# Performance work log

Measured on AMD Instinct MI355X. Metric: run time of the kernel, lower is better.

## Reference

```python
import jax, jax.numpy as jnp
import numpy as np
import math

B, L, D = 4, 4096, 1024
PI = math.pi
LN_EPS = 1e-5


def setup_inputs() -> dict:
    key = jax.random.key(0)
    ks = jax.random.split(key, 16)
    s = 1.0 / math.sqrt(D)
    inp = {
        "x": jax.random.normal(ks[0], (B, L, D), dtype=jnp.float32),
        # Linear weights stored as [in, out] (torch W.T)
        "Wk": jax.random.normal(ks[1], (D, D), dtype=jnp.float32) * s,
        "bk": jnp.zeros((D,), dtype=jnp.float32),
        "Wq": jax.random.normal(ks[2], (D, D), dtype=jnp.float32) * s,
        "bq": jnp.zeros((D,), dtype=jnp.float32),
        "Wv": jax.random.normal(ks[3], (D, D), dtype=jnp.float32) * s,
        "bv": jnp.zeros((D,), dtype=jnp.float32),
        "ln_g": jnp.ones((D,), dtype=jnp.float32),
        "ln_b": jnp.zeros((D,), dtype=jnp.float32),
        "Wo": jax.random.normal(ks[4], (D, D), dtype=jnp.float32) * s,
        "bo": jnp.zeros((D,), dtype=jnp.float32),
        "Wg1": jax.random.normal(ks[5], (D, D // 4), dtype=jnp.float32) * s,
        "bg1": jnp.zeros((D // 4,), dtype=jnp.float32),
        "Wg2": jax.random.normal(ks[6], (D // 4, 1), dtype=jnp.float32) * (2.0 / math.sqrt(D)),
        "bg2": jnp.zeros((1,), dtype=jnp.float32),
        "pos_phases": jax.random.normal(ks[7], (L, D), dtype=jnp.float32) * PI,
    }
    return inp


def _layernorm(x, g, b):
    mu = jnp.mean(x, axis=-1, keepdims=True)
    var = jnp.var(x, axis=-1, keepdims=True)
    return (x - mu) * jax.lax.rsqrt(var + LN_EPS) * g + b


def reference(x, Wk, bk, Wq, bq, Wv, bv, ln_g, ln_b, Wo, bo, Wg1, bg1, Wg2, bg2, pos_phases):
    # dropout is identity in eval mode
    key_phases = jnp.tanh(x @ Wk + bk) * PI          # [B,L,D]
    query_phases = jnp.tanh(x @ Wq + bq) * PI        # [B,L,D]
    V = x @ Wv + bv                                   # [B,L,D]

    cos_k, sin_k = jnp.cos(key_phases), jnp.sin(key_phases)
    cos_q, sin_q = jnp.cos(query_phases), jnp.sin(query_phases)

    mem_real = jnp.cumsum(V * cos_k, axis=1)
    mem_imag = jnp.cumsum(V * sin_k, axis=1)
    content_retrieved = mem_real * cos_q + mem_imag * sin_q

    pp = pos_phases[: x.shape[1]]                     # [L,D]
    cos_p, sin_p = jnp.cos(pp), jnp.sin(pp)
    pos_mem_real = jnp.cumsum(V * cos_p, axis=1)
    pos_mem_imag = jnp.cumsum(V * sin_p, axis=1)
    pos_retrieved = pos_mem_real * cos_p + pos_mem_imag * sin_p

    gate = jax.nn.sigmoid(jax.nn.gelu(x @ Wg1 + bg1) @ Wg2 + bg2)  # [B,L,1]
    combined = gate * content_retrieved + (1.0 - gate) * pos_retrieved

    positions = jnp.arange(1, x.shape[1] + 1, dtype=jnp.float32)
    norm = jnp.sqrt(positions)[None, :, None]
    out = _layernorm(combined / norm, ln_g, ln_b) @ Wo + bo
    return x + out
```

## Files before the change

### kernel.cpp

```cpp
#include <hip/hip_runtime.h>
#include <math.h>

#define B_ 4
#define L_ 4096
#define D_ 1024
#define DG_ 256
#define NC_ 128
#define CL_ 32
#define PI_F 3.14159265358979323846f
#define LN_EPS_F 1e-5f

typedef __attribute__((ext_vector_type(8))) _Float16 f16x8;
typedef __attribute__((ext_vector_type(8))) short s16x8;
typedef __attribute__((ext_vector_type(4))) short s16x4;
typedef __attribute__((ext_vector_type(4))) float f32x4;

__device__ inline short f2h(float f) { return __builtin_bit_cast(short, (_Float16)f); }
__device__ inline float h2f(short s) { return (float)__builtin_bit_cast(_Float16, s); }

__device__ inline float ftanh(float x) {
    float e = __expf(2.0f * x);
    return 1.0f - 2.0f / (e + 1.0f);
}
__device__ inline void fsincos(float x, float* s, float* c) {
    *s = __sinf(x); *c = __cosf(x);
}

__device__ inline void gld16(const void* g, void* l) {
    __builtin_amdgcn_global_load_lds(
        (const __attribute__((address_space(1))) unsigned int*)g,
        (__attribute__((address_space(3))) unsigned int*)l, 16, 0, 0);
}

__global__ __launch_bounds__(256)
void conv_x(const float* __restrict__ x, short* __restrict__ xh, int n8)
{
    int t = blockIdx.x * 256 + threadIdx.x;
    if (t >= n8) return;
    const float4* p = (const float4*)x + (size_t)t * 2;
    float4 a = p[0], b = p[1];
    s16x8 v;
    v[0] = f2h(a.x); v[1] = f2h(a.y); v[2] = f2h(a.z); v[3] = f2h(a.w);
    v[4] = f2h(b.x); v[5] = f2h(b.y); v[6] = f2h(b.z); v[7] = f2h(b.w);
    *(s16x8*)(xh + (size_t)t * 8) = v;
}

__global__ __launch_bounds__(256)
void convT(const float* __restrict__ W, short* __restrict__ Th, int N)
{
    __shared__ float tile[64][65];
    const int n0 = blockIdx.x * 64, k0 = blockIdx.y * 64;
    const int t = threadIdx.x;
    const int r = t >> 4, c4 = (t & 15) * 4;

    #pragma unroll
    for (int i = 0; i < 4; ++i) {
        float4 v = *(const float4*)&W[(size_t)(k0 + r + i * 16) * N + n0 + c4];
        tile[r + i * 16][c4 + 0] = v.x;
        tile[r + i * 16][c4 + 1] = v.y;
        tile[r + i * 16][c4 + 2] = v.z;
        tile[r + i * 16][c4 + 3] = v.w;
    }
    __syncthreads();
    #pragma unroll
    for (int i = 0; i < 4; ++i) {
        const int n = r + i * 16;
        s16x4 o;
        o[0] = f2h(tile[c4 + 0][n]);
        o[1] = f2h(tile[c4 + 1][n]);
        o[2] = f2h(tile[c4 + 2][n]);
        o[3] = f2h(tile[c4 + 3][n]);
        *(s16x4*)&Th[(size_t)(n0 + n) * 1024 + k0 + c4] = o;
    }
}

__device__ inline f16x8 ldf(const char* lds, int ofs, int r, int colb) {
    return *(const f16x8*)(lds + ofs + r * 128 + (colb ^ ((r & 7) << 4)));
}

#define STG(srcp, rbase, kt, lofs)                                              \
    gld16((const char*)(srcp) + (size_t)((rbase) + sr) * (size_t)(K * 2) +      \
              (kt) * 128 + sc,                                                  \
          lds + (lofs) + (w << 10))

#define MFMA_Q(MG, NG)                                                          \
    _Pragma("unroll") for (int i_ = 0; i_ < 4; ++i_)                            \
    _Pragma("unroll") for (int j_ = 0; j_ < 2; ++j_)                            \
    _Pragma("unroll") for (int kk_ = 0; kk_ < 2; ++kk_)                         \
        acc[(MG)*4 + i_][(NG)*2 + j_] = __builtin_amdgcn_mfma_f32_16x16x32_f16( \
            af[i_][kk_], bq[NG][j_][kk_], acc[(MG)*4 + i_][(NG)*2 + j_], 0, 0, 0);

#define SBAR() __builtin_amdgcn_sched_barrier(0)

template<int EPI, typename OT>
__global__ __launch_bounds__(512, 2)
void mgemm256(const short* __restrict__ A, const short* __restrict__ Bt,
              const float* __restrict__ X, OT* __restrict__ out0,
              short* __restrict__ out1, short* __restrict__ out2,
              const float* __restrict__ b0, const float* __restrict__ b1,
              const float* __restrict__ b2, int M, int N, int K)
{
    extern __shared__ char lds[];

    const int tid = threadIdx.x;
    const int w = tid >> 6, l = tid & 63;
    const int wr = w >> 2, wc = w & 3;
    const int fr = l & 15, kb = l >> 4;
    const int bm = blockIdx.x * 256, bn = blockIdx.y * 256;
    const int nt = K >> 6;

    const int p0 = tid * 16;
    const int sr = p0 >> 7;
    const int sc = (p0 & 127) ^ ((sr & 7) << 4);

    f32x4 acc[8][4] = {};
    f16x8 af[4][2];
    f16x8 bq[2][2][2];

    STG(A, bm +   0, 0, 0);             STG(A, bm + 128, 0, 16384);
    STG(A, bm +  64, 0, 8192);          STG(A, bm + 192, 0, 16384 + 8192);
    STG(Bt, bn +   0, 0, 32768);        STG(Bt, bn +  64, 0, 32768 + 8192);
    STG(Bt, bn + 128, 0, 32768 + 16384);STG(Bt, bn + 192, 0, 32768 + 16384 + 8192);
    STG(A, bm +   0, 1, 65536);         STG(A, bm + 128, 1, 65536 + 16384);
    STG(A, bm +  64, 1, 65536 + 8192);  STG(A, bm + 192, 1, 65536 + 16384 + 8192);
    STG(Bt, bn +   0, 1, 98304);        STG(Bt, bn +  64, 1, 98304 + 8192);
    STG(Bt, bn + 128, 1, 98304 + 16384);STG(Bt, bn + 192, 1, 98304 + 16384 + 8192);
    asm volatile("s_waitcnt vmcnt(8)" ::: "memory");
    SBAR(); __builtin_amdgcn_s_barrier(); SBAR();

    for (int t = 0; t < nt; ++t) {
        const int Ab = (t & 1) << 16, Bb = Ab + 32768;
        const int An = ((t & 1) ^ 1) << 16, Bn = An + 32768;
        const bool sNext = (t >= 1) && (t + 1 < nt);
        const bool sAF   = (t + 2 < nt);

        #pragma unroll
        for (int i = 0; i < 4; ++i)
            #pragma unroll
            for (int kk = 0; kk < 2; ++kk)
                af[i][kk] = ldf(lds, Ab + (wr << 14), i * 16 + fr, (kk << 6) + (kb << 4));
        #pragma unroll
        for (int j = 0; j < 2; ++j)
            #pragma unroll
            for (int kk = 0; kk < 2; ++kk)
                bq[0][j][kk] = ldf(lds, Bb + ((wc >> 1) << 14),
                                   ((wc & 1) << 6) + j * 16 + fr, (kk << 6) + (kb << 4));
        if (sNext) { STG(A, bm + 64, t + 1, An + 8192); STG(A, bm + 192, t + 1, An + 16384 + 8192); }
        SBAR(); __builtin_amdgcn_s_barrier(); SBAR();
        __builtin_amdgcn_s_setprio(1);
        MFMA_Q(0, 0);
        __builtin_amdgcn_s_setprio(0);
        SBAR(); __builtin_amdgcn_s_barrier(); SBAR();

        #pragma unroll
        for (int j = 0; j < 2; ++j)
            #pragma unroll
            for (int kk = 0; kk < 2; ++kk)
                bq[1][j][kk] = ldf(lds, Bb + ((wc >> 1) << 14),
                                   ((wc & 1) << 6) + (2 + j) * 16 + fr, (kk << 6) + (kb << 4));
        if (sNext) { STG(Bt, bn + 0, t + 1, Bn); STG(Bt, bn + 64, t + 1, Bn + 8192); }
        SBAR(); __builtin_amdgcn_s_barrier(); SBAR();
        __builtin_amdgcn_s_setprio(1);
        MFMA_Q(0, 1);
        __builtin_amdgcn_s_setprio(0);
        SBAR(); __builtin_amdgcn_s_barrier(); SBAR();

        #pragma unroll
        for (int i = 0; i < 4; ++i)
            #pragma unroll
            for (int kk = 0; kk < 2; ++kk)
                af[i][kk] = ldf(lds, Ab + (wr << 14), (4 + i) * 16 + fr, (kk << 6) + (kb << 4));
        if (sNext) { STG(Bt, bn + 128, t + 1, Bn + 16384); STG(Bt, bn + 192, t + 1, Bn + 16384 + 8192); }
        SBAR(); __builtin_amdgcn_s_barrier(); SBAR();
        __builtin_amdgcn_s_setprio(1);
        MFMA_Q(1, 0);
        __builtin_amdgcn_s_setprio(0);
        SBAR(); __builtin_amdgcn_s_barrier(); SBAR();

        if (sAF) { STG(A, bm + 0, t + 2, Ab); STG(A, bm + 128, t + 2, Ab + 16384); }
        SBAR(); __builtin_amdgcn_s_barrier(); SBAR();
        __builtin_amdgcn_s_setprio(1);
        MFMA_Q(1, 1);
        __builtin_amdgcn_s_setprio(0);
        SBAR();
        if (t < nt - 1) {
            if (sAF) { asm volatile("s_waitcnt vmcnt(2)" ::: "memory"); }
            else     { asm volatile("s_waitcnt vmcnt(0)" ::: "memory"); }
            __builtin_amdgcn_s_barrier(); SBAR();
        }
    }

    if constexpr (EPI == 4) {
        short* op; const float* bp; bool dt;
        if (bn < 1024)      { op = (short*)out0; bp = b0; dt = true;  }
        else if (bn < 2048) { op = out1;         bp = b1; dt = true;  }
        else                { op = out2;         bp = b2; dt = false; }
        const int cb = bn & 1023;
        #pragma unroll
        for (int nf = 0; nf < 4; ++nf) {
            const int cc = cb + wc * 64 + nf * 16 + fr;
            const float bcol = bp[cc];
            #pragma unroll
            for (int mf = 0; mf < 8; ++mf)
                #pragma unroll
                for (int rr = 0; rr < 4; ++rr) {
                    const int row = bm + wr * 128 + mf * 16 + kb * 4 + rr;
                    float c = acc[mf][nf][rr] + bcol;
                    if (dt) c = ftanh(c) * PI_F;
                    op[(size_t)row * 1024 + cc] = f2h(c);
                }
        }
    } else {
        #pragma unroll
        for (int nf = 0; nf < 4; ++nf) {
            const int col = bn + wc * 64 + nf * 16 + fr;
            const float bcol = b0[col];
            #pragma unroll
            for (int mf = 0; mf < 8; ++mf)
                #pragma unroll
                for (int rr = 0; rr < 4; ++rr) {
                    const int row = bm + wr * 128 + mf * 16 + kb * 4 + rr;
                    float c = acc[mf][nf][rr] + bcol + X[(size_t)row * N + col];
                    ((float*)out0)[(size_t)row * N + col] = c;
                }
        }
    }
}

template<int EPI>
__global__ __launch_bounds__(256)
void mgemm(const short* __restrict__ A, const short* __restrict__ Bt,
           short* __restrict__ out0, const float* __restrict__ b0,
           int M, int N, int K)
{
    __shared__ __align__(16) short As[128 * 32];
    __shared__ __align__(16) short Bs[128 * 32];

    const int tid = threadIdx.x;
    const int w  = tid >> 6, l = tid & 63;
    const int wr = w >> 1,  wc = w & 1;
    const int fr = l & 15,  kb = l >> 4;
    const int bm = blockIdx.x * 128, bn = blockIdx.y * 128;

    const int srow = l >> 2;
    const int scol = (l & 3) * 8;
    const short* gA0 = A  + (size_t)(bm + w * 32 +  0 + srow) * K + scol;
    const short* gA1 = A  + (size_t)(bm + w * 32 + 16 + srow) * K + scol;
    const short* gB0 = Bt + (size_t)(bn + w * 32 +  0 + srow) * K + scol;
    const short* gB1 = Bt + (size_t)(bn + w * 32 + 16 + srow) * K + scol;
    short* lA0 = &As[(w * 32 +  0) * 32];
    short* lA1 = &As[(w * 32 + 16) * 32];
    short* lB0 = &Bs[(w * 32 +  0) * 32];
    short* lB1 = &Bs[(w * 32 + 16) * 32];

    f32x4 acc[4][4] = {};

    for (int k0 = 0; k0 < K; k0 += 32) {
        gld16(gA0 + k0, lA0); gld16(gA1 + k0, lA1);
        gld16(gB0 + k0, lB0); gld16(gB1 + k0, lB1);
        __syncthreads();

        f16x8 afr[4], bfr[4];
        #pragma unroll
        for (int m = 0; m < 4; ++m)
            afr[m] = *(const f16x8*)&As[(wr * 64 + m * 16 + fr) * 32 + kb * 8];
        #pragma unroll
        for (int n = 0; n < 4; ++n)
            bfr[n] = *(const f16x8*)&Bs[(wc * 64 + n * 16 + fr) * 32 + kb * 8];
        #pragma unroll
        for (int m = 0; m < 4; ++m)
            #pragma unroll
            for (int n = 0; n < 4; ++n)
                acc[m][n] = __builtin_amdgcn_mfma_f32_16x16x32_f16(afr[m], bfr[n], acc[m][n], 0, 0, 0);
        __syncthreads();
    }

    #pragma unroll
    for (int n = 0; n < 4; ++n) {
        const int col = bn + wc * 64 + n * 16 + fr;
        const float bcol = b0[col];
        #pragma unroll
        for (int m = 0; m < 4; ++m)
            #pragma unroll
            for (int r = 0; r < 4; ++r) {
                const int row = bm + wr * 64 + m * 16 + kb * 4 + r;
                float c = acc[m][n][r] + bcol;
                float tt = 0.7978845608028654f * (c + 0.044715f * c * c * c);
                c = 0.5f * c * (1.0f + ftanh(tt));
                out0[(size_t)row * N + col] = f2h(c);
            }
    }
}

__global__ __launch_bounds__(256)
void gate_kernel(const short* __restrict__ H, const float* __restrict__ Wg2,
                 const float* __restrict__ bg2, float* __restrict__ gate)
{
    const int wid = threadIdx.x >> 6;
    const int lane = threadIdx.x & 63;
    const int row = blockIdx.x * 4 + wid;
    s16x4 hv = *(const s16x4*)&H[(size_t)row * DG_ + lane * 4];
    float4 wv = *(const float4*)&Wg2[lane * 4];
    float s = h2f(hv[0]) * wv.x + h2f(hv[1]) * wv.y + h2f(hv[2]) * wv.z + h2f(hv[3]) * wv.w;
    #pragma unroll
    for (int o = 32; o; o >>= 1) s += __shfl_down(s, o);
    if (lane == 0) gate[row] = 1.0f / (1.0f + __expf(-(s + bg2[0])));
}

__global__ __launch_bounds__(256)
void passA(const short* __restrict__ V, const short* __restrict__ KP,
           const float* __restrict__ PP, f32x4* __restrict__ SI)
{
    const int bid = blockIdx.x;
    const int b = bid >> 7, c = bid & 127;
    const int d0 = threadIdx.x * 4;

    f32x4 cr = {}, ci = {}, pr = {}, pi = {};
    const size_t base  = ((size_t)b * L_ + (size_t)c * CL_) * D_ + d0;
    const size_t pbase = (size_t)c * CL_ * D_ + d0;
    for (int ll = 0; ll < CL_; ++ll) {
        s16x4 v4  = *(const s16x4*)&V [base + (size_t)ll * D_];
        s16x4 kp4 = *(const s16x4*)&KP[base + (size_t)ll * D_];
        f32x4 pp4 = *(const f32x4*)&PP[pbase + (size_t)ll * D_];
        #pragma unroll
        for (int j = 0; j < 4; ++j) {
            float v = h2f(v4[j]);
            float sk, ck, sp, cp;
            fsincos(h2f(kp4[j]), &sk, &ck);
            fsincos(pp4[j], &sp, &cp);
            cr[j] += v * ck; ci[j] += v * sk;
            pr[j] += v * cp; pi[j] += v * sp;
        }
    }
    const size_t sidx = ((size_t)bid << 10) + d0;
    #pragma unroll
    for (int j = 0; j < 4; ++j) {
        f32x4 o = { cr[j], ci[j], pr[j], pi[j] };
        SI[sidx + j] = o;
    }
}

__global__ __launch_bounds__(256)
void passB(f32x4* __restrict__ SI)
{
    const int t = blockIdx.x * 256 + threadIdx.x;
    const int b = t >> 10, d = t & 1023;
    f32x4 run = {};
    for (int c = 0; c < NC_; ++c) {
        const size_t idx = ((size_t)(b * NC_ + c) << 10) + d;
        f32x4 v = SI[idx];
        SI[idx] = run;
        run += v;
    }
}

__global__ __launch_bounds__(256)
void passC(const short* __restrict__ V, const short* KP,
           const short* __restrict__ QP, const float* __restrict__ PP,
           const float* __restrict__ gate, const f32x4* __restrict__ SI,
           const float* __restrict__ ln_g, const float* __restrict__ ln_b,
           short* Yb)
{
    const int bid = blockIdx.x;
    const int b = bid >> 7, c = bid & 127;
    const int d0 = threadIdx.x * 4;

    const size_t sidx = ((size_t)bid << 10) + d0;
    f32x4 cr, ci, pr, pi;
    #pragma unroll
    for (int j = 0; j < 4; ++j) {
        f32x4 s = SI[sidx + j];
        cr[j] = s[0]; ci[j] = s[1]; pr[j] = s[2]; pi[j] = s[3];
    }
    const f32x4 g_ln = *(const f32x4*)&ln_g[d0];
    const f32x4 b_ln = *(const f32x4*)&ln_b[d0];

    __shared__ float2 lred[2][4];
    const int wid = threadIdx.x >> 6;
    const int lane = threadIdx.x & 63;

    for (int l0 = 0; l0 < CL_; ++l0) {
        const int ll = c * CL_ + l0;
        const size_t off = ((size_t)b * L_ + ll) * D_ + d0;
        s16x4 v4  = *(const s16x4*)&V [off];
        s16x4 kp4 = *(const s16x4*)&KP[off];
        s16x4 qp4 = *(const s16x4*)&QP[off];
        f32x4 pp4 = *(const f32x4*)&PP[(size_t)ll * D_ + d0];
        const float gv = gate[b * L_ + ll];
        const float rs_pos = rsqrtf((float)(ll + 1));

        f32x4 u;
        #pragma unroll
        for (int j = 0; j < 4; ++j) {
            float v = h2f(v4[j]);
            float sk, ck, sq, cq, sp, cp;
            fsincos(h2f(kp4[j]), &sk, &ck);
            fsincos(h2f(qp4[j]), &sq, &cq);
            fsincos(pp4[j], &sp, &cp);
            cr[j] += v * ck; ci[j] += v * sk;
            pr[j] += v * cp; pi[j] += v * sp;
            float content = cr[j] * cq + ci[j] * sq;
            float posr    = pr[j] * cp + pi[j] * sp;
            u[j] = (gv * content + (1.0f - gv) * posr) * rs_pos;
        }

        float s  = u[0] + u[1] + u[2] + u[3];
        float s2 = u[0]*u[0] + u[1]*u[1] + u[2]*u[2] + u[3]*u[3];
        #pragma unroll
        for (int o = 32; o; o >>= 1) {
            s  += __shfl_down(s, o);
            s2 += __shfl_down(s2, o);
        }
        const int pb = l0 & 1;
        if (lane == 0) lred[pb][wid] = make_float2(s, s2);
        __syncthreads();
        float ts  = lred[pb][0].x + lred[pb][1].x + lred[pb][2].x + lred[pb][3].x;
        float ts2 = lred[pb][0].y + lred[pb][1].y + lred[pb][2].y + lred[pb][3].y;
        const float mu  = ts * (1.0f / D_);
        const float var = ts2 * (1.0f / D_) - mu * mu;
        const float rsv = rsqrtf(var + LN_EPS_F);
        s16x4 yo;
        #pragma unroll
        for (int j = 0; j < 4; ++j)
            yo[j] = f2h((u[j] - mu) * rsv * g_ln[j] + b_ln[j]);
        *(s16x4*)&Yb[off] = yo;
    }
}

extern "C" void kernel_launch(void* const* d_in, const int* in_sizes, int n_in,
                              void* d_out, int out_size, void* d_ws, size_t ws_size,
                              hipStream_t stream)
{
    const float* x    = (const float*)d_in[0];
    const float* Wk   = (const float*)d_in[1];
    const float* bk   = (const float*)d_in[2];
    const float* Wq   = (const float*)d_in[3];
    const float* bq   = (const float*)d_in[4];
    const float* Wv   = (const float*)d_in[5];
    const float* bv   = (const float*)d_in[6];
    const float* ln_g = (const float*)d_in[7];
    const float* ln_b = (const float*)d_in[8];
    const float* Wo   = (const float*)d_in[9];
    const float* bo   = (const float*)d_in[10];
    const float* Wg1  = (const float*)d_in[11];
    const float* bg1  = (const float*)d_in[12];
    const float* Wg2  = (const float*)d_in[13];
    const float* bg2  = (const float*)d_in[14];
    const float* PP   = (const float*)d_in[15];

    float* out = (float*)d_out;

    const size_t BLD   = (size_t)B_ * L_ * D_;
    const size_t SZ_X  = BLD * 2;
    const size_t SZ_R1 = (size_t)B_ * L_ * DG_ * 2;
    const size_t SZ_G1 = (size_t)D_ * DG_ * 2;
    const size_t NEED  = SZ_X + SZ_R1 + SZ_G1 + 3 * SZ_X;
    if (ws_size < NEED) {
        hipMemcpyAsync(d_out, d_in[0], BLD * sizeof(float),
                       hipMemcpyDeviceToDevice, stream);
        return;
    }

    char* wsb = (char*)d_ws;
    short* xh   = (short*)(wsb);
    char*  r1   = wsb + SZ_X;
    short* Wcat = (short*)r1;
    short* H    = (short*)r1;
    short* Wg1T = (short*)(r1 + SZ_R1);
    short* KP   = (short*)(r1 + SZ_R1 + SZ_G1);
    short* QP   = (short*)((char*)KP + SZ_X);
    short* V    = (short*)((char*)QP + SZ_X);
    float* gate = (float*)(wsb);
    short* WtO  = (short*)(wsb + 65536);
    f32x4* SI   = (f32x4*)(wsb + 65536 + 2097152);
    short* Yb   = KP;

    const int M = B_ * L_;
    dim3 blk(256);

    conv_x<<<(int)(BLD / 8 / 256), blk, 0, stream>>>(x, xh, (int)(BLD / 8));
    dim3 gT(D_ / 64, 16);
    dim3 gTg(DG_ / 64, 16);
    convT<<<gT, blk, 0, stream>>>(Wk, Wcat + 0 * D_ * D_, D_);
    convT<<<gT, blk, 0, stream>>>(Wq, Wcat + 1 * D_ * D_, D_);
    convT<<<gT, blk, 0, stream>>>(Wv, Wcat + 2 * D_ * D_, D_);
    convT<<<gTg, blk, 0, stream>>>(Wg1, Wg1T, DG_);

    dim3 gQKV(M / 256, 3072 / 256);
    dim3 gH(M / 128, DG_ / 128);
    hipLaunchKernelGGL((mgemm256<4, short>), gQKV, dim3(512), 131072, stream,
                       xh, Wcat, nullptr, KP, QP, V, bk, bq, bv, M, 3072, D_);
    hipLaunchKernelGGL((mgemm<2>), gH, blk, 0, stream,
                       xh, Wg1T, H, bg1, M, DG_, D_);

    gate_kernel<<<M / 4, blk, 0, stream>>>(H, Wg2, bg2, gate);
    convT<<<gT, blk, 0, stream>>>(Wo, WtO, D_);

    passA<<<B_ * NC_, blk, 0, stream>>>(V, KP, PP, SI);
    passB<<<(B_ * D_) / 256, blk, 0, stream>>>(SI);
    passC<<<B_ * NC_, blk, 0, stream>>>(V, KP, QP, PP, gate, SI, ln_g, ln_b, Yb);

    dim3 gO(M / 256, D_ / 256);
    hipLaunchKernelGGL((mgemm256<3, float>), gO, dim3(512), 131072, stream,
                       Yb, WtO, x, out, nullptr, nullptr, bo, nullptr, nullptr,
                       M, D_, D_);
}
```

Measured before the change: 328.4 us.

## Restructure GEMM main loop into two-tile unrolled phases with precomputed LDS pointers

Rewrites the mgemm256 K-loop to process two 64-wide K tiles per iteration with a static double-buffer schedule. LDS fragment addresses are precomputed as base pointers plus immediate offsets, so the per-load XOR swizzle arithmetic goes away. All four B fragments are loaded at once, which cuts each tile from four MFMA phases to two and halves the barriers per tile. Global loads are rescheduled around these phases. In exchange, more B fragments stay live in registers, and the hand-written load ordering and vmcnt counts must match exactly.

```diff
diff --git a/kernel.cpp b/kernel.cpp
--- a/kernel.cpp
+++ b/kernel.cpp
@@ -74,23 +74,26 @@
     }
 }
 
-__device__ inline f16x8 ldf(const char* lds, int ofs, int r, int colb) {
-    return *(const f16x8*)(lds + ofs + r * 128 + (colb ^ ((r & 7) << 4)));
-}
-
-#define STG(srcp, rbase, kt, lofs)                                              \
-    gld16((const char*)(srcp) + (size_t)((rbase) + sr) * (size_t)(K * 2) +      \
-              (kt) * 128 + sc,                                                  \
-          lds + (lofs) + (w << 10))
-
-#define MFMA_Q(MG, NG)                                                          \
-    _Pragma("unroll") for (int i_ = 0; i_ < 4; ++i_)                            \
-    _Pragma("unroll") for (int j_ = 0; j_ < 2; ++j_)                            \
-    _Pragma("unroll") for (int kk_ = 0; kk_ < 2; ++kk_)                         \
-        acc[(MG)*4 + i_][(NG)*2 + j_] = __builtin_amdgcn_mfma_f32_16x16x32_f16( \
-            af[i_][kk_], bq[NG][j_][kk_], acc[(MG)*4 + i_][(NG)*2 + j_], 0, 0, 0);
-
 #define SBAR() __builtin_amdgcn_sched_barrier(0)
+#define BARRIER() do { SBAR(); __builtin_amdgcn_s_barrier(); SBAR(); } while (0)
+#define LDH(P, IMM) (*(const f16x8*)((P) + (IMM)))
+
+#define RD_AF(BASEIMM)                                                  \
+    _Pragma("unroll") for (int i_ = 0; i_ < 4; ++i_) {                  \
+        af[i_][0] = LDH(Ak0, (BASEIMM) + i_ * 2048);                    \
+        af[i_][1] = LDH(Ak1, (BASEIMM) + i_ * 2048);                    \
+    }
+#define RD_BQ(BASEIMM)                                                  \
+    _Pragma("unroll") for (int n_ = 0; n_ < 4; ++n_) {                  \
+        bq[n_][0] = LDH(Bk0, (BASEIMM) + n_ * 2048);                    \
+        bq[n_][1] = LDH(Bk1, (BASEIMM) + n_ * 2048);                    \
+    }
+#define MFMAS(MG)                                                       \
+    _Pragma("unroll") for (int i_ = 0; i_ < 4; ++i_)                    \
+    _Pragma("unroll") for (int n_ = 0; n_ < 4; ++n_)                    \
+    _Pragma("unroll") for (int kk_ = 0; kk_ < 2; ++kk_)                 \
+        acc[(MG) * 4 + i_][n_] = __builtin_amdgcn_mfma_f32_16x16x32_f16(\
+            af[i_][kk_], bq[n_][kk_], acc[(MG) * 4 + i_][n_], 0, 0, 0);
 
 template<int EPI, typename OT>
 __global__ __launch_bounds__(512, 2)
@@ -107,87 +110,93 @@
     const int wr = w >> 2, wc = w & 3;
     const int fr = l & 15, kb = l >> 4;
     const int bm = blockIdx.x * 256, bn = blockIdx.y * 256;
-    const int nt = K >> 6;
+    const int np = K >> 7;
+
+    const int s = fr & 7;
+    const int cK0 = (((s >> 2) & 1) << 6) | (((kb ^ s) & 3) << 4);
+    const char* Ak0 = lds + (wr << 14) + fr * 128 + cK0;
+    const char* Ak1 = lds + (wr << 14) + fr * 128 + (cK0 ^ 64);
+    const char* Bk0 = lds + 32768 + ((wc >> 1) << 14) + ((wc & 1) * 64 + fr) * 128 + cK0;
+    const char* Bk1 = lds + 32768 + ((wc >> 1) << 14) + ((wc & 1) * 64 + fr) * 128 + (cK0 ^ 64);
 
     const int p0 = tid * 16;
     const int sr = p0 >> 7;
     const int sc = (p0 & 127) ^ ((sr & 7) << 4);
+    const short* gA = A  + (size_t)(bm + sr) * K + (sc >> 1);
+    const short* gB = Bt + (size_t)(bn + sr) * K + (sc >> 1);
+    char* ldst = lds + (w << 10);
+    const size_t q1 = (size_t)64 * K, q2 = 2 * q1, q3 = 3 * q1;
 
     f32x4 acc[8][4] = {};
     f16x8 af[4][2];
-    f16x8 bq[2][2][2];
-
-    STG(A, bm +   0, 0, 0);             STG(A, bm + 128, 0, 16384);
-    STG(A, bm +  64, 0, 8192);          STG(A, bm + 192, 0, 16384 + 8192);
-    STG(Bt, bn +   0, 0, 32768);        STG(Bt, bn +  64, 0, 32768 + 8192);
-    STG(Bt, bn + 128, 0, 32768 + 16384);STG(Bt, bn + 192, 0, 32768 + 16384 + 8192);
-    STG(A, bm +   0, 1, 65536);         STG(A, bm + 128, 1, 65536 + 16384);
-    STG(A, bm +  64, 1, 65536 + 8192);  STG(A, bm + 192, 1, 65536 + 16384 + 8192);
-    STG(Bt, bn +   0, 1, 98304);        STG(Bt, bn +  64, 1, 98304 + 8192);
-    STG(Bt, bn + 128, 1, 98304 + 16384);STG(Bt, bn + 192, 1, 98304 + 16384 + 8192);
-    asm volatile("s_waitcnt vmcnt(8)" ::: "memory");
-    SBAR(); __builtin_amdgcn_s_barrier(); SBAR();
-
-    for (int t = 0; t < nt; ++t) {
-        const int Ab = (t & 1) << 16, Bb = Ab + 32768;
-        const int An = ((t & 1) ^ 1) << 16, Bn = An + 32768;
-        const bool sNext = (t >= 1) && (t + 1 < nt);
-        const bool sAF   = (t + 2 < nt);
-
-        #pragma unroll
-        for (int i = 0; i < 4; ++i)
-            #pragma unroll
-            for (int kk = 0; kk < 2; ++kk)
-                af[i][kk] = ldf(lds, Ab + (wr << 14), i * 16 + fr, (kk << 6) + (kb << 4));
-        #pragma unroll
-        for (int j = 0; j < 2; ++j)
-            #pragma unroll
-            for (int kk = 0; kk < 2; ++kk)
-                bq[0][j][kk] = ldf(lds, Bb + ((wc >> 1) << 14),
-                                   ((wc & 1) << 6) + j * 16 + fr, (kk << 6) + (kb << 4));
-        if (sNext) { STG(A, bm + 64, t + 1, An + 8192); STG(A, bm + 192, t + 1, An + 16384 + 8192); }
-        SBAR(); __builtin_amdgcn_s_barrier(); SBAR();
-        __builtin_amdgcn_s_setprio(1);
-        MFMA_Q(0, 0);
-        __builtin_amdgcn_s_setprio(0);
-        SBAR(); __builtin_amdgcn_s_barrier(); SBAR();
-
-        #pragma unroll
-        for (int j = 0; j < 2; ++j)
-            #pragma unroll
-            for (int kk = 0; kk < 2; ++kk)
-                bq[1][j][kk] = ldf(lds, Bb + ((wc >> 1) << 14),
-                                   ((wc & 1) << 6) + (2 + j) * 16 + fr, (kk << 6) + (kb << 4));
-        if (sNext) { STG(Bt, bn + 0, t + 1, Bn); STG(Bt, bn + 64, t + 1, Bn + 8192); }
-        SBAR(); __builtin_amdgcn_s_barrier(); SBAR();
-        __builtin_amdgcn_s_setprio(1);
-        MFMA_Q(0, 1);
-        __builtin_amdgcn_s_setprio(0);
-        SBAR(); __builtin_amdgcn_s_barrier(); SBAR();
-
-        #pragma unroll
-        for (int i = 0; i < 4; ++i)
-            #pragma unroll
-            for (int kk = 0; kk < 2; ++kk)
-                af[i][kk] = ldf(lds, Ab + (wr << 14), (4 + i) * 16 + fr, (kk << 6) + (kb << 4));
-        if (sNext) { STG(Bt, bn + 128, t + 1, Bn + 16384); STG(Bt, bn + 192, t + 1, Bn + 16384 + 8192); }
-        SBAR(); __builtin_amdgcn_s_barrier(); SBAR();
-        __builtin_amdgcn_s_setprio(1);
-        MFMA_Q(1, 0);
-        __builtin_amdgcn_s_setprio(0);
-        SBAR(); __builtin_amdgcn_s_barrier(); SBAR();
-
-        if (sAF) { STG(A, bm + 0, t + 2, Ab); STG(A, bm + 128, t + 2, Ab + 16384); }
-        SBAR(); __builtin_amdgcn_s_barrier(); SBAR();
-        __builtin_amdgcn_s_setprio(1);
-        MFMA_Q(1, 1);
-        __builtin_amdgcn_s_setprio(0);
+    f16x8 bq[4][2];
+
+    gld16(gA,       ldst);
+    gld16(gA + q1,  ldst + 8192);
+    gld16(gA + q2,  ldst + 16384);
+    gld16(gA + q3,  ldst + 24576);
+    gld16(gB,       ldst + 32768);
+    gld16(gB + q1,  ldst + 40960);
+    gld16(gB + q2,  ldst + 49152);
+    gld16(gB + q3,  ldst + 57344);
+    gld16(gA +      64, ldst + 65536);
+    gld16(gA + q2 + 64, ldst + 65536 + 16384);
+    asm volatile("s_waitcnt vmcnt(2)" ::: "memory");
+    BARRIER();
+
+    const short* gA1 = gA + 64;
+    const short* gB1 = gB + 64;
+
+    for (int pp = 0; pp < np; ++pp) {
+        const bool nl = (pp + 1 < np);
+
+        RD_AF(0); RD_BQ(0);
+        gld16(gA1 + q1, ldst + 65536 + 8192);
+        gld16(gA1 + q3, ldst + 65536 + 24576);
+        gld16(gB1,      ldst + 65536 + 32768);
+        gld16(gB1 + q1, ldst + 65536 + 40960);
+        BARRIER();
+        __builtin_amdgcn_s_setprio(1); MFMAS(0); __builtin_amdgcn_s_setprio(0);
+        BARRIER();
+        RD_AF(8192);
+        gld16(gB1 + q2, ldst + 65536 + 49152);
+        gld16(gB1 + q3, ldst + 65536 + 57344);
+        if (nl) {
+            gld16(gA1 +      64, ldst);
+            gld16(gA1 + q2 + 64, ldst + 16384);
+        }
+        BARRIER();
+        __builtin_amdgcn_s_setprio(1); MFMAS(1); __builtin_amdgcn_s_setprio(0);
         SBAR();
-        if (t < nt - 1) {
-            if (sAF) { asm volatile("s_waitcnt vmcnt(2)" ::: "memory"); }
-            else     { asm volatile("s_waitcnt vmcnt(0)" ::: "memory"); }
+        if (nl) asm volatile("s_waitcnt vmcnt(2)" ::: "memory");
+        else    asm volatile("s_waitcnt vmcnt(0)" ::: "memory");
+        __builtin_amdgcn_s_barrier(); SBAR();
+
+        RD_AF(65536); RD_BQ(65536);
+        if (nl) {
+            gld16(gA1 + q1 + 64, ldst + 8192);
+            gld16(gA1 + q3 + 64, ldst + 24576);
+            gld16(gB1 +      64, ldst + 32768);
+            gld16(gB1 + q1 + 64, ldst + 40960);
+        }
+        BARRIER();
+        __builtin_amdgcn_s_setprio(1); MFMAS(0); __builtin_amdgcn_s_setprio(0);
+        BARRIER();
+        RD_AF(65536 + 8192);
+        if (nl) {
+            gld16(gB1 + q2 + 64, ldst + 49152);
+            gld16(gB1 + q3 + 64, ldst + 57344);
+            gld16(gA1 +      128, ldst + 65536);
+            gld16(gA1 + q2 + 128, ldst + 65536 + 16384);
+        }
+        BARRIER();
+        __builtin_amdgcn_s_setprio(1); MFMAS(1); __builtin_amdgcn_s_setprio(0);
+        SBAR();
+        if (nl) {
+            asm volatile("s_waitcnt vmcnt(2)" ::: "memory");
             __builtin_amdgcn_s_barrier(); SBAR();
         }
+        gA1 += 128; gB1 += 128;
     }
 
     if constexpr (EPI == 4) {
```

After: 326.1 us. Within noise of the previous version (-0.7%).
